# Performance work log

Measured on AMD Instinct MI355X. Metric: run time of the kernel, lower is better.

Reference implementation:

```python
import jax, jax.numpy as jnp
import numpy as np

THETA = 10000.0


def apply_rope(t):
    """Partial rotary on first head_dim//2 dims, interleaved pairs (rotary_embedding_torch).
    t: (B, H, S, D) float32."""
    B, H, S, D = t.shape
    rot_dim = D // 2  # RotaryEmbedding(head_dim // 2)
    inv_freq = 1.0 / (THETA ** (jnp.arange(0, rot_dim, 2, dtype=jnp.float32) / rot_dim))  # (rot_dim//2,)
    pos = jnp.arange(S, dtype=jnp.float32)
    freqs = pos[:, None] * inv_freq[None, :]            # (S, rot_dim//2)
    freqs = jnp.repeat(freqs, 2, axis=-1)               # (S, rot_dim) interleaved
    cos, sin = jnp.cos(freqs), jnp.sin(freqs)           # (S, rot_dim)
    t_rot, t_pass = t[..., :rot_dim], t[..., rot_dim:]
    x1 = t_rot[..., 0::2]
    x2 = t_rot[..., 1::2]
    rot_half = jnp.stack((-x2, x1), axis=-1).reshape(t_rot.shape)
    t_rot = t_rot * cos + rot_half * sin
    return jnp.concatenate([t_rot, t_pass], axis=-1)


def setup_inputs() -> dict:
    key = jax.random.key(0)
    k1, k2, k3, k4, k5 = jax.random.split(key, 5)
    B, S, Dm = 2, 2048, 1024
    scale = 1.0 / np.sqrt(Dm)
    return {
        "x": jax.random.normal(k1, (B, S, Dm), dtype=jnp.float32),
        "Wqkv": jax.random.normal(k2, (3 * Dm, Dm), dtype=jnp.float32) * scale,
        "bqkv": jax.random.normal(k3, (3 * Dm,), dtype=jnp.float32) * 0.01,
        "Wout": jax.random.normal(k4, (Dm, Dm), dtype=jnp.float32) * scale,
        "bout": jax.random.normal(k5, (Dm,), dtype=jnp.float32) * 0.01,
    }


def reference(x, Wqkv, bqkv, Wout, bout):
    B, S, Dm = x.shape
    H = 16
    Dh = Dm // H
    qkv = x @ Wqkv.T + bqkv                              # (B, S, 3*Dm)
    qkv = qkv.reshape(B, S, 3, H, Dh).transpose(2, 0, 3, 1, 4)  # (3, B, H, S, Dh)
    q, k, v = qkv[0], qkv[1], qkv[2]
    q = apply_rope(q.astype(jnp.float32))
    k = apply_rope(k.astype(jnp.float32))
    scores = jnp.einsum("bhqd,bhkd->bhqk", q, k) / jnp.sqrt(jnp.float32(Dh))
    attn = jax.nn.softmax(scores, axis=-1)
    out = jnp.einsum("bhqk,bhkd->bhqd", attn, v)         # (B, H, S, Dh)
    out = out.transpose(0, 2, 1, 3).reshape(B, S, Dm)
    return out @ Wout.T + bout
```

## Files before the change

kernel.cpp:

```cpp
#include <hip/hip_runtime.h>

#define S_LEN 2048
#define DMODEL 1024
#define NHEAD 16
#define DHEAD 64
#define BATCH 2
#define BH_TOT (BATCH * NHEAD)
#define TOK (BATCH * S_LEN)
#define NQKV (3 * DMODEL)

#define QSCALE 0.18033688011112042f

typedef float  f32x4  __attribute__((ext_vector_type(4)));
typedef __bf16 bf16x8 __attribute__((ext_vector_type(8)));
typedef __bf16 bf16x4 __attribute__((ext_vector_type(4)));
typedef __bf16 bf16x2 __attribute__((ext_vector_type(2)));
typedef short  s16x4  __attribute__((ext_vector_type(4)));

typedef __attribute__((address_space(1))) void* as1_ptr;
typedef __attribute__((address_space(3))) void* as3_ptr;

__device__ __forceinline__ void gl2lds16(const void* g, void* l) {
  __builtin_amdgcn_global_load_lds((as1_ptr)(void*)g, (as3_ptr)l, 16, 0, 0);
}

__device__ __forceinline__ f32x4 mfma32(bf16x8 a, bf16x8 b, f32x4 c) {
  return __builtin_amdgcn_mfma_f32_16x16x32_bf16(a, b, c, 0, 0, 0);
}
__device__ __forceinline__ f32x4 mfma16(bf16x4 a, bf16x4 b, f32x4 c) {
  return __builtin_amdgcn_mfma_f32_16x16x16bf16_1k(
      __builtin_bit_cast(s16x4, a), __builtin_bit_cast(s16x4, b), c, 0, 0, 0);
}

__global__ __launch_bounds__(256) void cvt_kernel(const float* __restrict__ src,
                                                  __bf16* __restrict__ dst, int n) {
  const int i = (blockIdx.x * 256 + threadIdx.x) * 4;
  if (i >= n) return;
  const f32x4 v = *(const f32x4*)(src + i);
  bf16x4 o;
  o[0] = (__bf16)v[0]; o[1] = (__bf16)v[1]; o[2] = (__bf16)v[2]; o[3] = (__bf16)v[3];
  *(bf16x4*)(dst + i) = o;
}

__device__ __forceinline__ void gemm_tile_128(const __bf16* __restrict__ A,
                                              const __bf16* __restrict__ Bw,
                                              const int Kd, const int tileM, const int tileN,
                                              __bf16* As, __bf16* Bs, f32x4 acc[4][4]) {
  const int t    = threadIdx.x;
  const int lane = t & 63;
  const int wave = t >> 6;
  const int quad = lane >> 4;
  const int c    = lane & 15;
  const int wm   = (wave >> 1) << 6;
  const int wn   = (wave & 1) << 6;

  const int u0 = t, u1 = t + 256;
  const __bf16* gA0 = A  + (size_t)(tileM + (u0 >> 2)) * Kd + (u0 & 3) * 8;
  const __bf16* gA1 = A  + (size_t)(tileM + (u1 >> 2)) * Kd + (u1 & 3) * 8;
  const __bf16* gB0 = Bw + (size_t)(tileN + (u0 >> 2)) * Kd + (u0 & 3) * 8;
  const __bf16* gB1 = Bw + (size_t)(tileN + (u1 >> 2)) * Kd + (u1 & 3) * 8;
  __bf16* lA0 = As + u0 * 8; __bf16* lA1 = As + u1 * 8;
  __bf16* lB0 = Bs + u0 * 8; __bf16* lB1 = Bs + u1 * 8;

  for (int k0 = 0; k0 < Kd; k0 += 32) {
    gl2lds16(gA0 + k0, lA0);
    gl2lds16(gA1 + k0, lA1);
    gl2lds16(gB0 + k0, lB0);
    gl2lds16(gB1 + k0, lB1);
    __syncthreads();
    bf16x8 af[4], bfr[4];
#pragma unroll
    for (int mt = 0; mt < 4; ++mt)
      af[mt] = *(const bf16x8*)(As + (wm + mt * 16 + c) * 32 + quad * 8);
#pragma unroll
    for (int nt = 0; nt < 4; ++nt)
      bfr[nt] = *(const bf16x8*)(Bs + (wn + nt * 16 + c) * 32 + quad * 8);
#pragma unroll
    for (int mt = 0; mt < 4; ++mt)
#pragma unroll
      for (int nt = 0; nt < 4; ++nt)
        acc[mt][nt] = mfma32(af[mt], bfr[nt], acc[mt][nt]);
    __syncthreads();
  }
}

__global__ __launch_bounds__(256) void gemm_qkv_kernel(const __bf16* __restrict__ xb,
                                                       const __bf16* __restrict__ Wb,
                                                       const float* __restrict__ bias,
                                                       __bf16* __restrict__ Qb,
                                                       __bf16* __restrict__ Kb,
                                                       __bf16* __restrict__ Vtb) {
  __shared__ __align__(16) __bf16 As[128 * 32];
  __shared__ __align__(16) __bf16 Bs[128 * 32];
  f32x4 acc[4][4];
#pragma unroll
  for (int i = 0; i < 4; ++i)
#pragma unroll
    for (int j = 0; j < 4; ++j) acc[i][j] = (f32x4){0.f, 0.f, 0.f, 0.f};

  const int tileM = blockIdx.y * 128;
  const int tileN = blockIdx.x * 128;
  gemm_tile_128(xb, Wb, DMODEL, tileM, tileN, As, Bs, acc);

  const int t = threadIdx.x;
  const int lane = t & 63, wave = t >> 6;
  const int quad = lane >> 4, c = lane & 15;
  const int wm = (wave >> 1) << 6, wn = (wave & 1) << 6;

#pragma unroll
  for (int nt = 0; nt < 4; ++nt) {
    const int col = tileN + wn + nt * 16 + c;
    const float bv = bias[col];
    const int which = col >> 10;
    const int h  = (col >> 6) & 15;
    const int dh = col & 63;
    if (which == 2) {
#pragma unroll
      for (int mt = 0; mt < 4; ++mt) {
        const int row0 = tileM + wm + mt * 16 + quad * 4;
        const int bb = row0 >> 11;
        const int ss = row0 & (S_LEN - 1);
        bf16x4 o;
#pragma unroll
        for (int r = 0; r < 4; ++r) o[r] = (__bf16)(acc[mt][nt][r] + bv);
        *(bf16x4*)(Vtb + (((size_t)(bb * NHEAD + h)) * DHEAD + dh) * S_LEN + ss) = o;
      }
    } else {
      __bf16* dst = (which == 0) ? Qb : Kb;
      const float scl = (which == 0) ? QSCALE : 1.0f;
#pragma unroll
      for (int mt = 0; mt < 4; ++mt) {
#pragma unroll
        for (int r = 0; r < 4; ++r) {
          const int row = tileM + wm + mt * 16 + quad * 4 + r;
          const int bb = row >> 11;
          const int ss = row & (S_LEN - 1);
          dst[(((size_t)(bb * NHEAD + h)) * S_LEN + ss) * DHEAD + dh] =
              (__bf16)((acc[mt][nt][r] + bv) * scl);
        }
      }
    }
  }
}

__global__ __launch_bounds__(256) void gemm_out_kernel(const __bf16* __restrict__ AOb,
                                                       const __bf16* __restrict__ Wb,
                                                       const float* __restrict__ bout,
                                                       float* __restrict__ out) {
  __shared__ __align__(16) __bf16 As[128 * 32];
  __shared__ __align__(16) __bf16 Bs[128 * 32];
  f32x4 acc[4][4];
#pragma unroll
  for (int i = 0; i < 4; ++i)
#pragma unroll
    for (int j = 0; j < 4; ++j) acc[i][j] = (f32x4){0.f, 0.f, 0.f, 0.f};

  const int tileM = blockIdx.y * 128;
  const int tileN = blockIdx.x * 128;
  gemm_tile_128(AOb, Wb, DMODEL, tileM, tileN, As, Bs, acc);

  const int t = threadIdx.x;
  const int lane = t & 63, wave = t >> 6;
  const int quad = lane >> 4, c = lane & 15;
  const int wm = (wave >> 1) << 6, wn = (wave & 1) << 6;

#pragma unroll
  for (int nt = 0; nt < 4; ++nt) {
    const int col = tileN + wn + nt * 16 + c;
    const float bv = bout[col];
#pragma unroll
    for (int mt = 0; mt < 4; ++mt) {
#pragma unroll
      for (int r = 0; r < 4; ++r) {
        const int row = tileM + wm + mt * 16 + quad * 4 + r;
        out[(size_t)row * DMODEL + col] = acc[mt][nt][r] + bv;
      }
    }
  }
}

__global__ __launch_bounds__(256) void rope_kernel(__bf16* __restrict__ Qb, __bf16* __restrict__ Kb) {
  const int idx = blockIdx.x * 256 + threadIdx.x;
  const int j  = idx & 15;
  const int s  = (idx >> 4) & (S_LEN - 1);
  const int bh = (idx >> 15) & (BH_TOT - 1);
  __bf16* base = (idx >> 20) ? Kb : Qb;
  bf16x2* p = (bf16x2*)(base + ((size_t)bh * S_LEN + s) * DHEAD) + j;
  bf16x2 v = *p;
  const float x1 = (float)v[0];
  const float x2 = (float)v[1];
  const float LOG2_10000 = 13.287712379549449f;
  const float inv = exp2f(-(float)j * (LOG2_10000 / 16.0f));
  const float ang = (float)s * inv;
  float sn, cs;
  sincosf(ang, &sn, &cs);
  bf16x2 o;
  o[0] = (__bf16)(x1 * cs - x2 * sn);
  o[1] = (__bf16)(x2 * cs + x1 * sn);
  *p = o;
}

__global__ __launch_bounds__(256, 2) void attn_kernel(const __bf16* __restrict__ Qb,
                                                      const __bf16* __restrict__ Kb,
                                                      const __bf16* __restrict__ Vtb,
                                                      __bf16* __restrict__ AOb) {
  __shared__ __align__(16) __bf16 Ks[2][64 * 64];
  __shared__ __align__(16) __bf16 Vts[2][64 * 64];

  const int qt = blockIdx.x;
  const int bh = blockIdx.y;
  const int b = bh >> 4, h = bh & 15;
  const int t = threadIdx.x, wave = t >> 6, lane = t & 63;
  const int quad = lane >> 4, c = lane & 15;
  const size_t head = (size_t)bh * S_LEN * DHEAD;
  const int q0w = qt * 128 + wave * 32;

  bf16x8 qf[2][2];
#pragma unroll
  for (int nq = 0; nq < 2; ++nq) {
    const __bf16* qp = Qb + head + (size_t)(q0w + nq * 16 + c) * DHEAD + quad * 8;
    qf[nq][0] = *(const bf16x8*)qp;
    qf[nq][1] = *(const bf16x8*)(qp + 32);
  }

  f32x4 ot[4][2];
#pragma unroll
  for (int dt = 0; dt < 4; ++dt)
#pragma unroll
    for (int nq = 0; nq < 2; ++nq) ot[dt][nq] = (f32x4){0.f, 0.f, 0.f, 0.f};
  float lp[2] = {0.f, 0.f};

  const int u0 = t, u1 = t + 256;
  const int r0 = u0 >> 3, ch0 = (u0 & 7) ^ (r0 & 7);
  const int r1 = u1 >> 3, ch1 = (u1 & 7) ^ (r1 & 7);
  const __bf16* kg0 = Kb + head + (size_t)r0 * DHEAD + ch0 * 8;
  const __bf16* kg1 = Kb + head + (size_t)r1 * DHEAD + ch1 * 8;
  const __bf16* vg0 = Vtb + ((size_t)bh * DHEAD + r0) * S_LEN + ch0 * 8;
  const __bf16* vg1 = Vtb + ((size_t)bh * DHEAD + r1) * S_LEN + ch1 * 8;

  gl2lds16(kg0, &Ks[0][u0 * 8]);
  gl2lds16(kg1, &Ks[0][u1 * 8]);
  gl2lds16(vg0, &Vts[0][u0 * 8]);
  gl2lds16(vg1, &Vts[0][u1 * 8]);

  const int cxor = c & 7;

  for (int kb = 0; kb < S_LEN / 64; ++kb) {
    __syncthreads();
    const int cur = kb & 1;
    if (kb + 1 < S_LEN / 64) {
      const int nxt = cur ^ 1;
      const int k0n = (kb + 1) * 64;
      gl2lds16(kg0 + (size_t)k0n * DHEAD, &Ks[nxt][u0 * 8]);
      gl2lds16(kg1 + (size_t)k0n * DHEAD, &Ks[nxt][u1 * 8]);
      gl2lds16(vg0 + k0n, &Vts[nxt][u0 * 8]);
      gl2lds16(vg1 + k0n, &Vts[nxt][u1 * 8]);
    }

    bf16x8 kA[4][2];
#pragma unroll
    for (int mt = 0; mt < 4; ++mt) {
      const int row = mt * 16 + c;
#pragma unroll
      for (int hh = 0; hh < 2; ++hh)
        kA[mt][hh] = *(const bf16x8*)(&Ks[cur][row * 64 + (((hh * 4 + quad) ^ cxor) * 8)]);
    }

    bf16x4 pf[2][4];
#pragma unroll
    for (int nq = 0; nq < 2; ++nq) {
#pragma unroll
      for (int mt = 0; mt < 4; ++mt) {
        f32x4 z = (f32x4){0.f, 0.f, 0.f, 0.f};
        z = mfma32(kA[mt][0], qf[nq][0], z);
        z = mfma32(kA[mt][1], qf[nq][1], z);
#pragma unroll
        for (int r = 0; r < 4; ++r) {
          const float p = __builtin_amdgcn_exp2f(z[r]);
          lp[nq] += p;
          pf[nq][mt][r] = (__bf16)p;
        }
      }
    }

#pragma unroll
    for (int dt = 0; dt < 4; ++dt) {
      const int drow = dt * 16 + c;
#pragma unroll
      for (int mt = 0; mt < 4; ++mt) {
        const int chl = (mt * 2 + (quad >> 1)) ^ cxor;
        const bf16x4 vA = *(const bf16x4*)(&Vts[cur][drow * 64 + chl * 8 + (quad & 1) * 4]);
#pragma unroll
        for (int nq = 0; nq < 2; ++nq)
          ot[dt][nq] = mfma16(vA, pf[nq][mt], ot[dt][nq]);
      }
    }
  }

#pragma unroll
  for (int nq = 0; nq < 2; ++nq) {
    float l = lp[nq];
    l += __shfl_xor(l, 16);
    l += __shfl_xor(l, 32);
    const float inv = 1.0f / l;
    const int q = q0w + nq * 16 + c;
#pragma unroll
    for (int dt = 0; dt < 4; ++dt) {
      bf16x4 o;
#pragma unroll
      for (int r = 0; r < 4; ++r) o[r] = (__bf16)(ot[dt][nq][r] * inv);
      *(bf16x4*)(AOb + ((size_t)(b * S_LEN + q)) * DMODEL + h * DHEAD + dt * 16 + quad * 4) = o;
    }
  }
}

extern "C" void kernel_launch(void* const* d_in, const int* in_sizes, int n_in,
                              void* d_out, int out_size, void* d_ws, size_t ws_size,
                              hipStream_t stream) {
  const float* x    = (const float*)d_in[0];
  const float* Wqkv = (const float*)d_in[1];
  const float* bqkv = (const float*)d_in[2];
  const float* Wout = (const float*)d_in[3];
  const float* bout = (const float*)d_in[4];
  float* out = (float*)d_out;

  char* ws = (char*)d_ws;
  __bf16* xb    = (__bf16*)(ws + 0);
  __bf16* Wqkvb = (__bf16*)(ws + (size_t)8  * 1024 * 1024);
  __bf16* Woutb = (__bf16*)(ws + (size_t)14 * 1024 * 1024);
  __bf16* Qb    = (__bf16*)(ws + (size_t)16 * 1024 * 1024);
  __bf16* Kb    = (__bf16*)(ws + (size_t)24 * 1024 * 1024);
  __bf16* Vtb   = (__bf16*)(ws + (size_t)32 * 1024 * 1024);
  __bf16* AOb   = (__bf16*)(ws + (size_t)40 * 1024 * 1024);

  cvt_kernel<<<(TOK * DMODEL) / 1024, 256, 0, stream>>>(x, xb, TOK * DMODEL);
  cvt_kernel<<<(NQKV * DMODEL) / 1024, 256, 0, stream>>>(Wqkv, Wqkvb, NQKV * DMODEL);
  cvt_kernel<<<(DMODEL * DMODEL) / 1024, 256, 0, stream>>>(Wout, Woutb, DMODEL * DMODEL);

  gemm_qkv_kernel<<<dim3(NQKV / 128, TOK / 128), 256, 0, stream>>>(xb, Wqkvb, bqkv, Qb, Kb, Vtb);

  rope_kernel<<<(2 * BH_TOT * S_LEN * 16) / 256, 256, 0, stream>>>(Qb, Kb);

  attn_kernel<<<dim3(S_LEN / 128, BH_TOT), 256, 0, stream>>>(Qb, Kb, Vtb, AOb);

  gemm_out_kernel<<<dim3(DMODEL / 128, TOK / 128), 256, 0, stream>>>(AOb, Woutb, bout, out);
}
```

Measured before the change: 200.7 us.

## Switch attention to 32x32x16 MFMA with cross-lane shuffled P fragments

Rewrites the attention inner loop to use 32x32x16 bf16 MFMA for both QK^T and PV instead of 16x16 tiles. Each wave now handles 32 query rows as one 32-wide tile. The P fragments are repacked between the two MFMA layouts with xor-32 lane shuffles. Two accumulator sets are used to break the dependency chains. This cuts MFMA instruction count and LDS fragment reads per key block, at the cost of extra shuffles and higher register pressure.

```diff
diff --git a/kernel.cpp b/kernel.cpp
--- a/kernel.cpp
+++ b/kernel.cpp
@@ -12,10 +12,11 @@
 #define QSCALE 0.18033688011112042f
 
 typedef float  f32x4  __attribute__((ext_vector_type(4)));
+typedef float  f32x16 __attribute__((ext_vector_type(16)));
+typedef int    i32x4  __attribute__((ext_vector_type(4)));
 typedef __bf16 bf16x8 __attribute__((ext_vector_type(8)));
 typedef __bf16 bf16x4 __attribute__((ext_vector_type(4)));
 typedef __bf16 bf16x2 __attribute__((ext_vector_type(2)));
-typedef short  s16x4  __attribute__((ext_vector_type(4)));
 
 typedef __attribute__((address_space(1))) void* as1_ptr;
 typedef __attribute__((address_space(3))) void* as3_ptr;
@@ -27,9 +28,35 @@
 __device__ __forceinline__ f32x4 mfma32(bf16x8 a, bf16x8 b, f32x4 c) {
   return __builtin_amdgcn_mfma_f32_16x16x32_bf16(a, b, c, 0, 0, 0);
 }
-__device__ __forceinline__ f32x4 mfma16(bf16x4 a, bf16x4 b, f32x4 c) {
-  return __builtin_amdgcn_mfma_f32_16x16x16bf16_1k(
-      __builtin_bit_cast(s16x4, a), __builtin_bit_cast(s16x4, b), c, 0, 0, 0);
+
+__device__ __forceinline__ f32x16 mfma3216(bf16x8 a, bf16x8 b, f32x16 c) {
+  return __builtin_amdgcn_mfma_f32_32x32x16_bf16(a, b, c, 0, 0, 0);
+}
+
+__device__ __forceinline__ unsigned pack2(float a, float b) {
+  bf16x2 t;
+  t[0] = (__bf16)a;
+  t[1] = (__bf16)b;
+  return __builtin_bit_cast(unsigned, t);
+}
+
+__device__ __forceinline__ bf16x8 pfrag8(int hi,
+                                         float a0, float a1, float a2, float a3,
+                                         float a4, float a5, float a6, float a7) {
+  const unsigned wA = pack2(a0, a1);
+  const unsigned wB = pack2(a2, a3);
+  const unsigned wC = pack2(a4, a5);
+  const unsigned wD = pack2(a6, a7);
+  const unsigned sA = (unsigned)__shfl_xor((int)wA, 32);
+  const unsigned sB = (unsigned)__shfl_xor((int)wB, 32);
+  const unsigned sC = (unsigned)__shfl_xor((int)wC, 32);
+  const unsigned sD = (unsigned)__shfl_xor((int)wD, 32);
+  const unsigned r0 = hi ? sC : wA;
+  const unsigned r1 = hi ? sD : wB;
+  const unsigned r2 = hi ? wC : sA;
+  const unsigned r3 = hi ? wD : sB;
+  const i32x4 w = {(int)r0, (int)r1, (int)r2, (int)r3};
+  return __builtin_bit_cast(bf16x8, w);
 }
 
 __global__ __launch_bounds__(256) void cvt_kernel(const float* __restrict__ src,
@@ -211,24 +238,23 @@
   const int bh = blockIdx.y;
   const int b = bh >> 4, h = bh & 15;
   const int t = threadIdx.x, wave = t >> 6, lane = t & 63;
-  const int quad = lane >> 4, c = lane & 15;
+  const int c31 = lane & 31, hi = lane >> 5;
+  const int cx = c31 & 7;
   const size_t head = (size_t)bh * S_LEN * DHEAD;
   const int q0w = qt * 128 + wave * 32;
 
-  bf16x8 qf[2][2];
-#pragma unroll
-  for (int nq = 0; nq < 2; ++nq) {
-    const __bf16* qp = Qb + head + (size_t)(q0w + nq * 16 + c) * DHEAD + quad * 8;
-    qf[nq][0] = *(const bf16x8*)qp;
-    qf[nq][1] = *(const bf16x8*)(qp + 32);
-  }
-
-  f32x4 ot[4][2];
-#pragma unroll
-  for (int dt = 0; dt < 4; ++dt)
-#pragma unroll
-    for (int nq = 0; nq < 2; ++nq) ot[dt][nq] = (f32x4){0.f, 0.f, 0.f, 0.f};
-  float lp[2] = {0.f, 0.f};
+  bf16x8 qf[4];
+#pragma unroll
+  for (int s = 0; s < 4; ++s)
+    qf[s] = *(const bf16x8*)(Qb + head + (size_t)(q0w + c31) * DHEAD + s * 16 + hi * 8);
+
+  f32x16 zzero;
+#pragma unroll
+  for (int i = 0; i < 16; ++i) zzero[i] = 0.f;
+
+  f32x16 ota[2], otb[2];
+  ota[0] = zzero; ota[1] = zzero; otb[0] = zzero; otb[1] = zzero;
+  float lp = 0.f;
 
   const int u0 = t, u1 = t + 256;
   const int r0 = u0 >> 3, ch0 = (u0 & 7) ^ (r0 & 7);
@@ -243,7 +269,8 @@
   gl2lds16(vg0, &Vts[0][u0 * 8]);
   gl2lds16(vg1, &Vts[0][u1 * 8]);
 
-  const int cxor = c & 7;
+#define VREAD(db, gch) \
+  (*(const bf16x8*)(&Vts[cur][((db) * 32 + c31) * 64 + ((((gch) + hi) ^ cx) * 8)]))
 
   for (int kb = 0; kb < S_LEN / 64; ++kb) {
     __syncthreads();
@@ -257,59 +284,64 @@
       gl2lds16(vg1 + k0n, &Vts[nxt][u1 * 8]);
     }
 
-    bf16x8 kA[4][2];
-#pragma unroll
-    for (int mt = 0; mt < 4; ++mt) {
-      const int row = mt * 16 + c;
-#pragma unroll
-      for (int hh = 0; hh < 2; ++hh)
-        kA[mt][hh] = *(const bf16x8*)(&Ks[cur][row * 64 + (((hh * 4 + quad) ^ cxor) * 8)]);
-    }
-
-    bf16x4 pf[2][4];
-#pragma unroll
-    for (int nq = 0; nq < 2; ++nq) {
-#pragma unroll
-      for (int mt = 0; mt < 4; ++mt) {
-        f32x4 z = (f32x4){0.f, 0.f, 0.f, 0.f};
-        z = mfma32(kA[mt][0], qf[nq][0], z);
-        z = mfma32(kA[mt][1], qf[nq][1], z);
-#pragma unroll
-        for (int r = 0; r < 4; ++r) {
-          const float p = __builtin_amdgcn_exp2f(z[r]);
-          lp[nq] += p;
-          pf[nq][mt][r] = (__bf16)p;
-        }
-      }
-    }
-
-#pragma unroll
-    for (int dt = 0; dt < 4; ++dt) {
-      const int drow = dt * 16 + c;
-#pragma unroll
-      for (int mt = 0; mt < 4; ++mt) {
-        const int chl = (mt * 2 + (quad >> 1)) ^ cxor;
-        const bf16x4 vA = *(const bf16x4*)(&Vts[cur][drow * 64 + chl * 8 + (quad & 1) * 4]);
-#pragma unroll
-        for (int nq = 0; nq < 2; ++nq)
-          ot[dt][nq] = mfma16(vA, pf[nq][mt], ot[dt][nq]);
-      }
-    }
-  }
-
-#pragma unroll
-  for (int nq = 0; nq < 2; ++nq) {
-    float l = lp[nq];
-    l += __shfl_xor(l, 16);
-    l += __shfl_xor(l, 32);
-    const float inv = 1.0f / l;
-    const int q = q0w + nq * 16 + c;
-#pragma unroll
-    for (int dt = 0; dt < 4; ++dt) {
+    bf16x8 kA0[4], kA1[4];
+#pragma unroll
+    for (int s = 0; s < 4; ++s) {
+      kA0[s] = *(const bf16x8*)(&Ks[cur][c31 * 64 + (((s * 2 + hi) ^ cx) * 8)]);
+      kA1[s] = *(const bf16x8*)(&Ks[cur][(32 + c31) * 64 + (((s * 2 + hi) ^ cx) * 8)]);
+    }
+
+    f32x16 z0 = zzero, z1 = zzero;
+#pragma unroll
+    for (int s = 0; s < 4; ++s) {
+      z0 = mfma3216(kA0[s], qf[s], z0);
+      z1 = mfma3216(kA1[s], qf[s], z1);
+    }
+
+    float p0[16], p1[16];
+#pragma unroll
+    for (int r = 0; r < 16; ++r) p0[r] = __builtin_amdgcn_exp2f(z0[r]);
+#pragma unroll
+    for (int r = 0; r < 16; ++r) p1[r] = __builtin_amdgcn_exp2f(z1[r]);
+
+    lp += (((p0[0] + p0[1]) + (p0[2] + p0[3])) + ((p0[4] + p0[5]) + (p0[6] + p0[7])))
+        + (((p0[8] + p0[9]) + (p0[10] + p0[11])) + ((p0[12] + p0[13]) + (p0[14] + p0[15])));
+    lp += (((p1[0] + p1[1]) + (p1[2] + p1[3])) + ((p1[4] + p1[5]) + (p1[6] + p1[7])))
+        + (((p1[8] + p1[9]) + (p1[10] + p1[11])) + ((p1[12] + p1[13]) + (p1[14] + p1[15])));
+
+    {
+      const bf16x8 f0 = pfrag8(hi, p0[0], p0[1], p0[2], p0[3], p0[4], p0[5], p0[6], p0[7]);
+      ota[0] = mfma3216(VREAD(0, 0), f0, ota[0]);
+      ota[1] = mfma3216(VREAD(1, 0), f0, ota[1]);
+      const bf16x8 f1 = pfrag8(hi, p0[8], p0[9], p0[10], p0[11], p0[12], p0[13], p0[14], p0[15]);
+      otb[0] = mfma3216(VREAD(0, 2), f1, otb[0]);
+      otb[1] = mfma3216(VREAD(1, 2), f1, otb[1]);
+    }
+    {
+      const bf16x8 f0 = pfrag8(hi, p1[0], p1[1], p1[2], p1[3], p1[4], p1[5], p1[6], p1[7]);
+      ota[0] = mfma3216(VREAD(0, 4), f0, ota[0]);
+      ota[1] = mfma3216(VREAD(1, 4), f0, ota[1]);
+      const bf16x8 f1 = pfrag8(hi, p1[8], p1[9], p1[10], p1[11], p1[12], p1[13], p1[14], p1[15]);
+      otb[0] = mfma3216(VREAD(0, 6), f1, otb[0]);
+      otb[1] = mfma3216(VREAD(1, 6), f1, otb[1]);
+    }
+  }
+#undef VREAD
+
+#pragma unroll
+  for (int i = 0; i < 16; ++i) { ota[0][i] += otb[0][i]; ota[1][i] += otb[1][i]; }
+  const float l = lp + __shfl_xor(lp, 32);
+  const float inv = 1.0f / l;
+  const int q = q0w + c31;
+#pragma unroll
+  for (int db = 0; db < 2; ++db) {
+#pragma unroll
+    for (int rg = 0; rg < 4; ++rg) {
       bf16x4 o;
 #pragma unroll
-      for (int r = 0; r < 4; ++r) o[r] = (__bf16)(ot[dt][nq][r] * inv);
-      *(bf16x4*)(AOb + ((size_t)(b * S_LEN + q)) * DMODEL + h * DHEAD + dt * 16 + quad * 4) = o;
+      for (int i = 0; i < 4; ++i) o[i] = (__bf16)(ota[db][rg * 4 + i] * inv);
+      const int d0 = db * 32 + rg * 8 + hi * 4;
+      *(bf16x4*)(AOb + ((size_t)(b * S_LEN + q)) * DMODEL + h * DHEAD + d0) = o;
     }
   }
 }
```

After: 204.5 us. Within noise of the previous version (+1.9%).
